# Optimization experiments

Measured on AMD Instinct MI355X. Metric: run time of the kernel, lower is better.

Reference implementation:

```python
import jax, jax.numpy as jnp
import numpy as np

IN_DIM = 16384; DM = 512; DEPTH = 4
DI = 1024   # d_inner = expand * d_model
DS = 16     # d_state
DC = 4      # d_conv
DR = 32     # dt_rank = ceil(d_model/16)
B = 4; L = 256


def setup_inputs() -> dict:
    key = jax.random.key(0)
    ks = jax.random.split(key, 12)
    g = lambda k, s, sc=0.02: jax.random.normal(k, s, jnp.float32) * sc
    return {
        "x": jax.random.normal(ks[0], (B, L, IN_DIM), jnp.float32),
        # top-level projections / norm
        "in_w": g(ks[1], (DM, IN_DIM)), "in_b": jnp.zeros((DM,), jnp.float32),
        "ln_g": jnp.ones((DM,), jnp.float32), "ln_b": jnp.zeros((DM,), jnp.float32),
        "out_w": g(ks[2], (IN_DIM, DM)), "out_b": jnp.zeros((IN_DIM,), jnp.float32),
        # stacked per-layer Mamba params (leading dim = DEPTH)
        "m_in_w": g(ks[3], (DEPTH, 2 * DI, DM)),
        "conv_w": g(ks[4], (DEPTH, DI, DC), 0.2),
        "conv_b": jnp.zeros((DEPTH, DI), jnp.float32),
        "xproj_w": g(ks[5], (DEPTH, DR + 2 * DS, DI)),
        "dt_w": g(ks[6], (DEPTH, DI, DR), 0.1),
        "dt_b": jax.random.uniform(ks[7], (DEPTH, DI), jnp.float32, -4.0, -2.0),
        "A_log": jnp.log(jnp.broadcast_to(jnp.arange(1, DS + 1, dtype=jnp.float32), (DEPTH, DI, DS))),
        "D_p": jnp.ones((DEPTH, DI), jnp.float32),
        "m_out_w": g(ks[8], (DEPTH, DM, DI)),
    }


def _mamba(h, iw, cw, cb, xw, dw, db, Alog, Dp, ow):
    """One Mamba block (no residual, matching bare mamba_ssm.Mamba)."""
    Bn, Ln, _ = h.shape
    xz = h @ iw.T                                  # [B,L,2*DI]
    xc, z = jnp.split(xz, 2, axis=-1)
    # causal depthwise conv1d, kernel DC, truncated to L
    xp = jnp.pad(xc, ((0, 0), (DC - 1, 0), (0, 0)))
    conv = cb
    for k in range(DC):
        conv = conv + xp[:, k:k + Ln, :] * cw[:, k]
    xc = jax.nn.silu(conv)                         # [B,L,DI]
    xdbl = xc @ xw.T                               # [B,L,DR+2*DS]
    dt, Bm, Cm = xdbl[..., :DR], xdbl[..., DR:DR + DS], xdbl[..., DR + DS:]
    dt = jax.nn.softplus(dt @ dw.T + db)           # [B,L,DI]
    A = -jnp.exp(Alog)                             # [DI,DS]
    dA = jnp.exp(dt[..., None] * A)                # [B,L,DI,DS]
    dBx = dt[..., None] * Bm[:, :, None, :] * xc[..., None]  # [B,L,DI,DS]

    def step(hst, inp):
        a, b, c = inp
        hst = a * hst + b
        return hst, jnp.einsum('bdn,bn->bd', hst, c)

    h0 = jnp.zeros((Bn, DI, DS), xc.dtype)
    _, ys = jax.lax.scan(step, h0, (dA.transpose(1, 0, 2, 3), dBx.transpose(1, 0, 2, 3), Cm.transpose(1, 0, 2)))
    y = ys.transpose(1, 0, 2) + xc * Dp            # [B,L,DI]
    y = y * jax.nn.silu(z)
    return y @ ow.T                                # [B,L,DM]


def reference(x, in_w, in_b, ln_g, ln_b, out_w, out_b, m_in_w, conv_w, conv_b, xproj_w, dt_w, dt_b, A_log, D_p, m_out_w):
    h = x @ in_w.T + in_b                          # [B,L,DM]
    for i in range(DEPTH):
        h = _mamba(h, m_in_w[i], conv_w[i], conv_b[i], xproj_w[i], dt_w[i], dt_b[i], A_log[i], D_p[i], m_out_w[i])
    hl = h[:, -1]                                  # [B,DM]
    mu = hl.mean(-1, keepdims=True)
    var = ((hl - mu) ** 2).mean(-1, keepdims=True)
    hn = (hl - mu) / jnp.sqrt(var + 1e-5) * ln_g + ln_b
    return hn @ out_w.T + out_b                    # [B,IN_DIM]
```

## Files before the change

### kernel.cpp

```cpp
#include <hip/hip_runtime.h>
#include <stdint.h>

#define DEV static __device__ __forceinline__

typedef __attribute__((ext_vector_type(8))) __bf16 bf16x8;
typedef __attribute__((ext_vector_type(4))) float f32x4;

DEV float bfs2f(unsigned short u) {
    union { unsigned int i; float f; } c; c.i = ((unsigned int)u) << 16; return c.f;
}
DEV unsigned short f2bf(float v) {
    union { __bf16 b; unsigned short u; } c; c.b = (__bf16)v; return c.u;
}

template<int TH, int BM, int BN, int BK, int AMODE, int BMODE, int EPI,
         int CSPLIT, int SWZ, int DBUF>
__global__ __launch_bounds__(TH) void gemm_k(
    const void* __restrict__ A0, const void* __restrict__ A1,
    const void* __restrict__ B0, const void* __restrict__ B1,
    const float* __restrict__ bias,
    float* __restrict__ C0, float* __restrict__ C1,
    int lda, int ldb, int ldc, int Klen, int pstride)
{
    constexpr int NWN = TH / 128;
    constexpr int FM = BM / 2 / 16;
    constexpr int FN = BN / NWN / 16;
    constexpr int KB = BK / 32;
    constexpr int GAF = (AMODE == 0) ? BM * BK / (TH * 4) : 1;
    constexpr int GAP = (AMODE == 1) ? BM * BK / (TH * 8) : 1;
    constexpr int GBF = (BMODE == 0) ? BN * BK / (TH * 4) : 1;
    constexpr int GBP = (BMODE == 1) ? BN * BK / (TH * 8) : 1;
    constexpr int BUFB = 2 * (BM + BN) * BK * 2;

    __shared__ __align__(16) char smem[(DBUF ? 2 : 1) * BUFB];

    int bx = blockIdx.x, by = blockIdx.y, bz = blockIdx.z;
    if (SWZ == 1) {
        int lin = blockIdx.x + gridDim.x * (blockIdx.y + gridDim.y * blockIdx.z);
        bz = lin & 7;
        int rest = lin >> 3;
        bx = rest % gridDim.x;
        by = rest / gridDim.x;
    } else if (SWZ == 2) {
        int lin = blockIdx.x + gridDim.x * blockIdx.y;
        int xcd = lin & 7, t = lin >> 3;
        int gpx = gridDim.y / 8;
        by = xcd * gpx + t % gpx;
        bx = t / gpx;
    }

    const int tid = threadIdx.x, lane = tid & 63;
    const int wid = tid >> 6;
    const int wm = wid & 1, wn = wid >> 1;
    const int q = lane >> 4, t16 = lane & 15;
    const int tileM = bx * BM, tileN = by * BN;
    const int kBase = bz * Klen, kEnd = kBase + Klen;
    float* C = C0 + (size_t)bz * pstride;

    f32x4 acc[FM][FN];
#pragma unroll
    for (int a = 0; a < FM; ++a)
#pragma unroll
        for (int b = 0; b < FN; ++b) acc[a][b] = f32x4{0.f, 0.f, 0.f, 0.f};

    float4 aF[GAF], bF[GBF];
    int4 aH[GAP], aL[GAP], bH[GBP], bL[GBP];

    auto loadA = [&](int k0) {
        if (AMODE == 0) {
            const float* A32 = (const float*)A0;
#pragma unroll
            for (int u = 0; u < GAF; ++u) {
                int idx = u * TH + tid;
                int r = idx / (BK / 4), c4 = idx % (BK / 4);
                aF[u] = *(const float4*)(A32 + (size_t)(tileM + r) * lda + k0 + c4 * 4);
            }
        } else {
            const unsigned short* Ah = (const unsigned short*)A0;
            const unsigned short* Al = (const unsigned short*)A1;
#pragma unroll
            for (int u = 0; u < GAP; ++u) {
                int idx = u * TH + tid;
                int r = idx / (BK / 8), c8 = idx % (BK / 8);
                size_t src = (size_t)(tileM + r) * lda + k0 + c8 * 8;
                aH[u] = *(const int4*)(Ah + src);
                aL[u] = *(const int4*)(Al + src);
            }
        }
    };
    auto loadB = [&](int k0) {
        if (BMODE == 0) {
            const float* B32 = (const float*)B0;
#pragma unroll
            for (int u = 0; u < GBF; ++u) {
                int idx = u * TH + tid;
                int r = idx / (BK / 4), c4 = idx % (BK / 4);
                bF[u] = *(const float4*)(B32 + (size_t)(tileN + r) * ldb + k0 + c4 * 4);
            }
        } else {
            const unsigned short* Bh = (const unsigned short*)B0;
            const unsigned short* Bl = (const unsigned short*)B1;
#pragma unroll
            for (int u = 0; u < GBP; ++u) {
                int idx = u * TH + tid;
                int r = idx / (BK / 8), c8 = idx % (BK / 8);
                size_t src = (size_t)(tileN + r) * ldb + k0 + c8 * 8;
                bH[u] = *(const int4*)(Bh + src);
                bL[u] = *(const int4*)(Bl + src);
            }
        }
    };
    auto storeA = [&](char* sAh, char* sAl) {
        if (AMODE == 0) {
#pragma unroll
            for (int u = 0; u < GAF; ++u) {
                int idx = u * TH + tid;
                int r = idx / (BK / 4), c4 = idx % (BK / 4);
                float vv[4] = {aF[u].x, aF[u].y, aF[u].z, aF[u].w};
                ushort4 hv, lv;
                unsigned short* hp = (unsigned short*)&hv;
                unsigned short* lp = (unsigned short*)&lv;
#pragma unroll
                for (int e = 0; e < 4; ++e) {
                    unsigned short hb = f2bf(vv[e]);
                    hp[e] = hb; lp[e] = f2bf(vv[e] - bfs2f(hb));
                }
                int off = (c4 / 8) * BM * 64 + r * 64 + (c4 & 7) * 8;
                *(ushort4*)(sAh + off) = hv;
                *(ushort4*)(sAl + off) = lv;
            }
        } else {
#pragma unroll
            for (int u = 0; u < GAP; ++u) {
                int idx = u * TH + tid;
                int r = idx / (BK / 8), c8 = idx % (BK / 8);
                int off = (c8 / 4) * BM * 64 + r * 64 + (c8 & 3) * 16;
                *(int4*)(sAh + off) = aH[u];
                *(int4*)(sAl + off) = aL[u];
            }
        }
    };
    auto storeB = [&](char* sBh, char* sBl) {
        if (BMODE == 0) {
#pragma unroll
            for (int u = 0; u < GBF; ++u) {
                int idx = u * TH + tid;
                int r = idx / (BK / 4), c4 = idx % (BK / 4);
                float vv[4] = {bF[u].x, bF[u].y, bF[u].z, bF[u].w};
                ushort4 hv, lv;
                unsigned short* hp = (unsigned short*)&hv;
                unsigned short* lp = (unsigned short*)&lv;
#pragma unroll
                for (int e = 0; e < 4; ++e) {
                    unsigned short hb = f2bf(vv[e]);
                    hp[e] = hb; lp[e] = f2bf(vv[e] - bfs2f(hb));
                }
                int off = (c4 / 8) * BN * 64 + r * 64 + (c4 & 7) * 8;
                *(ushort4*)(sBh + off) = hv;
                *(ushort4*)(sBl + off) = lv;
            }
        } else {
#pragma unroll
            for (int u = 0; u < GBP; ++u) {
                int idx = u * TH + tid;
                int r = idx / (BK / 8), c8 = idx % (BK / 8);
                int off = (c8 / 4) * BN * 64 + r * 64 + (c8 & 3) * 16;
                *(int4*)(sBh + off) = bH[u];
                *(int4*)(sBl + off) = bL[u];
            }
        }
    };
    auto compute = [&](const char* sAh, const char* sAl,
                       const char* sBh, const char* sBl) {
#pragma unroll
        for (int kb = 0; kb < KB; ++kb) {
            bf16x8 ah[FM], al[FM], bh[FN], bl[FN];
#pragma unroll
            for (int fm = 0; fm < FM; ++fm) {
                int off = kb * BM * 64 + (wm * (BM / 2) + fm * 16 + t16) * 64 + q * 16;
                ah[fm] = *(const bf16x8*)(sAh + off);
                al[fm] = *(const bf16x8*)(sAl + off);
            }
#pragma unroll
            for (int fn = 0; fn < FN; ++fn) {
                int off = kb * BN * 64 + (wn * (BN / NWN) + fn * 16 + t16) * 64 + q * 16;
                bh[fn] = *(const bf16x8*)(sBh + off);
                bl[fn] = *(const bf16x8*)(sBl + off);
            }
#pragma unroll
            for (int fm = 0; fm < FM; ++fm)
#pragma unroll
                for (int fn = 0; fn < FN; ++fn) {
                    acc[fm][fn] = __builtin_amdgcn_mfma_f32_16x16x32_bf16(ah[fm], bh[fn], acc[fm][fn], 0, 0, 0);
                    acc[fm][fn] = __builtin_amdgcn_mfma_f32_16x16x32_bf16(al[fm], bh[fn], acc[fm][fn], 0, 0, 0);
                    acc[fm][fn] = __builtin_amdgcn_mfma_f32_16x16x32_bf16(ah[fm], bl[fn], acc[fm][fn], 0, 0, 0);
                }
        }
    };

    loadA(kBase); loadB(kBase);
    if (DBUF) {
        storeA(smem, smem + BM * BK * 2);
        storeB(smem + 2 * BM * BK * 2, smem + 2 * BM * BK * 2 + BN * BK * 2);
        __syncthreads();
        int p = 0;
        for (int k0 = kBase; k0 < kEnd; k0 += BK) {
            bool more = (k0 + BK < kEnd);
            if (more) { loadA(k0 + BK); loadB(k0 + BK); }
            char* cb = smem + p * BUFB;
            compute(cb, cb + BM * BK * 2,
                    cb + 2 * BM * BK * 2, cb + 2 * BM * BK * 2 + BN * BK * 2);
            if (more) {
                char* nb = smem + (p ^ 1) * BUFB;
                storeA(nb, nb + BM * BK * 2);
                storeB(nb + 2 * BM * BK * 2, nb + 2 * BM * BK * 2 + BN * BK * 2);
            }
            __syncthreads();
            p ^= 1;
        }
    } else {
        for (int k0 = kBase; k0 < kEnd; k0 += BK) {
            storeA(smem, smem + BM * BK * 2);
            storeB(smem + 2 * BM * BK * 2, smem + 2 * BM * BK * 2 + BN * BK * 2);
            __syncthreads();
            if (k0 + BK < kEnd) { loadA(k0 + BK); loadB(k0 + BK); }
            compute(smem, smem + BM * BK * 2,
                    smem + 2 * BM * BK * 2, smem + 2 * BM * BK * 2 + BN * BK * 2);
            __syncthreads();
        }
    }

#pragma unroll
    for (int fm = 0; fm < FM; ++fm) {
        int row0 = tileM + wm * (BM / 2) + fm * 16 + q * 4;
#pragma unroll
        for (int fn = 0; fn < FN; ++fn) {
            int col = tileN + wn * (BN / NWN) + fn * 16 + t16;
            float* Cd = C; int cc2 = col;
            if (CSPLIT && col >= ldc) { Cd = C1; cc2 = col - ldc; }
            float bv = (EPI == 2) ? bias[col] : 0.f;
#pragma unroll
            for (int r = 0; r < 4; ++r) {
                float v = acc[fm][fn][r];
                if (EPI == 2) { v = fminf(v + bv, 60.f); v = log1pf(__expf(v)); }
                Cd[(size_t)(row0 + r) * ldc + cc2] = v;
            }
        }
    }
}

__global__ __launch_bounds__(256) void reduce_k(
    const float* __restrict__ part, int Z, int pstride, int n,
    const float* __restrict__ bias, int colmask,
    unsigned short* __restrict__ hi, unsigned short* __restrict__ lo,
    float* __restrict__ hlast, int colbits)
{
    int i = blockIdx.x * 256 + threadIdx.x;
    if (i >= n) return;
    float s = 0.f;
    for (int z = 0; z < Z; ++z) s += part[(size_t)z * pstride + i];
    if (bias) s += bias[i & colmask];
    unsigned short hb = f2bf(s);
    hi[i] = hb; lo[i] = f2bf(s - bfs2f(hb));
    if (hlast) {
        int row = i >> colbits;
        if ((row & 255) == 255)
            hlast[((row >> 8) << colbits) + (i & colmask)] = s;
    }
}

__global__ __launch_bounds__(256) void conv_silu_k(
    const float* __restrict__ xb, const float* __restrict__ cw,
    const float* __restrict__ cb, unsigned short* __restrict__ xch,
    unsigned short* __restrict__ xcl)
{
    int i  = blockIdx.x * 256 + threadIdx.x;
    int d  = i & 1023;
    int bl = i >> 10;
    int l  = bl & 255;
    float a = cb[d];
#pragma unroll
    for (int k = 0; k < 4; ++k) {
        int ls = l + k - 3;
        if (ls >= 0) a += xb[(size_t)(bl + k - 3) * 1024 + d] * cw[d * 4 + k];
    }
    float v = a / (1.f + __expf(-a));
    unsigned short hb = f2bf(v);
    xch[i] = hb; xcl[i] = f2bf(v - bfs2f(hb));
}

__global__ __launch_bounds__(256) void scan_k(
    const float* __restrict__ zb,
    const unsigned short* __restrict__ xch, const unsigned short* __restrict__ xcl,
    const unsigned short* __restrict__ xdh, const unsigned short* __restrict__ xdl,
    const float* __restrict__ dt, const float* __restrict__ Alog,
    const float* __restrict__ Dp,
    unsigned short* __restrict__ ygh, unsigned short* __restrict__ ygl)
{
    __shared__ float sdt[2048], sxc[2048], szz[2048], sbc[2048];
    int b   = blockIdx.x >> 5;
    int d0  = (blockIdx.x & 31) << 5;
    int ch  = threadIdx.x >> 3;
    int d   = d0 + ch;
    int sub = threadIdx.x & 7;
    int j0  = sub * 2;
    float An[2], hst[2] = {0.f, 0.f};
    An[0] = -__expf(Alog[d * 16 + j0]);
    An[1] = -__expf(Alog[d * 16 + j0 + 1]);
    float Dd  = Dp[d];
    int   bl0 = b * 256;

    for (int c = 0; c < 4; ++c) {
        __syncthreads();
#pragma unroll
        for (int it = 0; it < 8; ++it) {
            int j2 = it * 256 + threadIdx.x;
            int ll = j2 >> 5, dd = j2 & 31;
            size_t row = (size_t)(bl0 + c * 64 + ll);
            size_t gi  = row * 1024 + d0 + dd;
            sdt[j2] = dt[gi];
            sxc[j2] = bfs2f(xch[gi]) + bfs2f(xcl[gi]);
            szz[j2] = zb[gi];
            size_t bi = row * 64 + 32 + dd;
            sbc[j2] = bfs2f(xdh[bi]) + bfs2f(xdl[bi]);
        }
        __syncthreads();
#pragma unroll 4
        for (int li = 0; li < 64; ++li) {
            float dtv = sdt[li * 32 + ch];
            float xcv = sxc[li * 32 + ch];
            float c1  = dtv * xcv;
            float dA0 = __expf(dtv * An[0]);
            float dA1 = __expf(dtv * An[1]);
            float B0  = sbc[li * 32 + j0],      B1 = sbc[li * 32 + j0 + 1];
            float C0  = sbc[li * 32 + 16 + j0], C1 = sbc[li * 32 + 16 + j0 + 1];
            hst[0] = dA0 * hst[0] + c1 * B0;
            hst[1] = dA1 * hst[1] + c1 * B1;
            float y = hst[0] * C0 + hst[1] * C1;
            y += __shfl_xor(y, 1);
            y += __shfl_xor(y, 2);
            y += __shfl_xor(y, 4);
            if (sub == 0) {
                float zv = szz[li * 32 + ch];
                float sg = zv / (1.f + __expf(-zv));
                float v  = (y + xcv * Dd) * sg;
                unsigned short hb = f2bf(v);
                size_t o = (size_t)(bl0 + c * 64 + li) * 1024 + d;
                ygh[o] = hb; ygl[o] = f2bf(v - bfs2f(hb));
            }
        }
    }
}

__global__ __launch_bounds__(512) void ln_k(
    const float* __restrict__ hlast, const float* __restrict__ g,
    const float* __restrict__ bb, float* __restrict__ hn)
{
    __shared__ float red[16];
    int b = blockIdx.x, k = threadIdx.x;
    float x = hlast[b * 512 + k];
    float s = x, s2 = x * x;
#pragma unroll
    for (int m = 32; m; m >>= 1) { s += __shfl_xor(s, m, 64); s2 += __shfl_xor(s2, m, 64); }
    if ((k & 63) == 0) { red[k >> 6] = s; red[8 + (k >> 6)] = s2; }
    __syncthreads();
    float ts = 0.f, ts2 = 0.f;
#pragma unroll
    for (int j = 0; j < 8; ++j) { ts += red[j]; ts2 += red[8 + j]; }
    float mu   = ts * (1.f / 512.f);
    float var  = ts2 * (1.f / 512.f) - mu * mu;
    float rstd = rsqrtf(var + 1e-5f);
    hn[b * 512 + k] = (x - mu) * rstd * g[k] + bb[k];
}

__global__ __launch_bounds__(256) void final_k(
    const float* __restrict__ hn, const float* __restrict__ W,
    const float* __restrict__ ob, float* __restrict__ out)
{
    int wid = threadIdx.x >> 6, lane = threadIdx.x & 63;
    float a[4][8];
#pragma unroll
    for (int b2 = 0; b2 < 4; ++b2) {
        float4 v0 = *(const float4*)&hn[b2 * 512 + lane * 8];
        float4 v1 = *(const float4*)&hn[b2 * 512 + lane * 8 + 4];
        a[b2][0] = v0.x; a[b2][1] = v0.y; a[b2][2] = v0.z; a[b2][3] = v0.w;
        a[b2][4] = v1.x; a[b2][5] = v1.y; a[b2][6] = v1.z; a[b2][7] = v1.w;
    }
#pragma unroll 1
    for (int it = 0; it < 8; ++it) {
        int n = blockIdx.x * 4 + wid + it * 2048;
        const float* W32 = W + (size_t)n * 512 + lane * 8;
        float4 v0 = *(const float4*)W32;
        float4 v1 = *(const float4*)(W32 + 4);
        float wf[8] = {v0.x, v0.y, v0.z, v0.w, v1.x, v1.y, v1.z, v1.w};
        float s0 = 0.f, s1 = 0.f, s2 = 0.f, s3 = 0.f;
#pragma unroll
        for (int j = 0; j < 8; ++j) {
            s0 += a[0][j] * wf[j]; s1 += a[1][j] * wf[j];
            s2 += a[2][j] * wf[j]; s3 += a[3][j] * wf[j];
        }
#pragma unroll
        for (int m = 32; m; m >>= 1) {
            s0 += __shfl_xor(s0, m, 64); s1 += __shfl_xor(s1, m, 64);
            s2 += __shfl_xor(s2, m, 64); s3 += __shfl_xor(s3, m, 64);
        }
        if (lane == 0) {
            float bv = ob[n];
            out[0 * 16384 + n] = s0 + bv;
            out[1 * 16384 + n] = s1 + bv;
            out[2 * 16384 + n] = s2 + bv;
            out[3 * 16384 + n] = s3 + bv;
        }
    }
}

extern "C" void kernel_launch(void* const* d_in, const int* in_sizes, int n_in,
                              void* d_out, int out_size, void* d_ws, size_t ws_size,
                              hipStream_t stream)
{
    const float* x      = (const float*)d_in[0];
    const float* in_w   = (const float*)d_in[1];
    const float* in_b   = (const float*)d_in[2];
    const float* ln_g   = (const float*)d_in[3];
    const float* ln_b   = (const float*)d_in[4];
    const float* out_w  = (const float*)d_in[5];
    const float* out_b  = (const float*)d_in[6];
    const float* m_in_w = (const float*)d_in[7];
    const float* conv_w = (const float*)d_in[8];
    const float* conv_b = (const float*)d_in[9];
    const float* xproj_w= (const float*)d_in[10];
    const float* dt_w   = (const float*)d_in[11];
    const float* dt_b   = (const float*)d_in[12];
    const float* A_log  = (const float*)d_in[13];
    const float* D_p    = (const float*)d_in[14];
    const float* m_out_w= (const float*)d_in[15];

    char* W = (char*)d_ws;
    unsigned short* hplh = (unsigned short*)(W + 0);
    unsigned short* hpll = (unsigned short*)(W + 1048576);
    float* hlast = (float*)(W + 2097152);
    float* hn    = (float*)(W + 2162688);
    float* xbuf  = (float*)(W + 2228224);
    float* zbuf  = (float*)(W + 6422528);
    unsigned short* xch = (unsigned short*)(W + 10616832);
    unsigned short* xcl = (unsigned short*)(W + 12713984);
    float* dtb   = (float*)(W + 14811136);
    unsigned short* xdbh  = (unsigned short*)(W + 19005440);
    unsigned short* xdbl_ = (unsigned short*)(W + 19136512);
    float* part1 = (float*)(W + 2228224);
    float* partx = (float*)(W + 14811136);
    float* parto = (float*)(W + 6422528);
    unsigned short* ygh = (unsigned short*)(W + 2228224);
    unsigned short* ygl = (unsigned short*)(W + 4325376);

    gemm_k<512,128,128,64,0,0,0,0,1,1><<<dim3(8,4,8),512,0,stream>>>(
        x, nullptr, in_w, nullptr, nullptr, part1, nullptr,
        16384, 16384, 512, 2048, 524288);
    reduce_k<<<2048,256,0,stream>>>(part1, 8, 524288, 524288, in_b, 511,
                                    hplh, hpll, hlast, 9);

    for (int i = 0; i < 4; ++i) {
        const float* iw = m_in_w  + (size_t)i * 1048576;
        const float* cw = conv_w  + (size_t)i * 4096;
        const float* cb = conv_b  + (size_t)i * 1024;
        const float* xw = xproj_w + (size_t)i * 65536;
        const float* dw = dt_w    + (size_t)i * 32768;
        const float* db = dt_b    + (size_t)i * 1024;
        const float* Al = A_log   + (size_t)i * 16384;
        const float* Dp = D_p     + (size_t)i * 1024;
        const float* ow = m_out_w + (size_t)i * 524288;

        gemm_k<512,64,128,64,1,0,0,1,2,0><<<dim3(16,16,1),512,0,stream>>>(
            hplh, hpll, iw, nullptr, nullptr, xbuf, zbuf, 512, 512, 1024, 512, 0);
        conv_silu_k<<<4096,256,0,stream>>>(xbuf, cw, cb, xch, xcl);
        gemm_k<256,64,64,64,1,0,0,0,0,0><<<dim3(16,1,16),256,0,stream>>>(
            xch, xcl, xw, nullptr, nullptr, partx, nullptr, 1024, 1024, 64, 64, 65536);
        reduce_k<<<256,256,0,stream>>>(partx, 16, 65536, 65536, nullptr, 63,
                                       xdbh, xdbl_, nullptr, 6);
        gemm_k<256,64,64,32,1,0,2,0,0,0><<<dim3(16,16,1),256,0,stream>>>(
            xdbh, xdbl_, dw, nullptr, db, dtb, nullptr, 64, 32, 1024, 32, 0);
        scan_k<<<128,256,0,stream>>>(zbuf, xch, xcl, xdbh, xdbl_, dtb, Al, Dp,
                                     ygh, ygl);
        gemm_k<512,64,128,64,1,0,0,0,1,0><<<dim3(16,4,8),512,0,stream>>>(
            ygh, ygl, ow, nullptr, nullptr, parto, nullptr, 1024, 1024, 512, 128, 524288);
        reduce_k<<<2048,256,0,stream>>>(parto, 8, 524288, 524288, nullptr, 511,
                                        hplh, hpll, hlast, 9);
    }

    ln_k<<<4,512,0,stream>>>(hlast, ln_g, ln_b, hn);
    final_k<<<512,256,0,stream>>>(hn, out_w, out_b, (float*)d_out);
}
```

Measured before the change: 765.0 us.

## Prefetch next scan chunk into registers; drop GEMM block swizzles and double buffering

The selective-scan kernel now loads the next 64-step chunk of dt, x, z and B/C from global memory into registers while the current chunk is processed, then writes it to shared memory between barriers. The aim is to hide global load latency behind the serial recurrence. Separately, the XCD-aware block swizzles (SWZ 1/2) are turned off for the in-projection and out-projection GEMMs, and the first large GEMM no longer uses LDS double buffering. Those GEMM changes trade possible L2 locality and overlap for simpler indexing and lower LDS use.

```diff
diff --git a/kernel.cpp b/kernel.cpp
--- a/kernel.cpp
+++ b/kernel.cpp
@@ -41,12 +41,6 @@
         int rest = lin >> 3;
         bx = rest % gridDim.x;
         by = rest / gridDim.x;
-    } else if (SWZ == 2) {
-        int lin = blockIdx.x + gridDim.x * blockIdx.y;
-        int xcd = lin & 7, t = lin >> 3;
-        int gpx = gridDim.y / 8;
-        by = xcd * gpx + t % gpx;
-        bx = t / gpx;
     }
 
     const int tid = threadIdx.x, lane = tid & 63;
@@ -310,21 +304,38 @@
     float Dd  = Dp[d];
     int   bl0 = b * 256;
 
-    for (int c = 0; c < 4; ++c) {
-        __syncthreads();
+    float rdt[8], rzz[8];
+    unsigned short rxh[8], rxl[8], rbh[8], rbl[8];
+    auto stage_load = [&](int c) {
 #pragma unroll
         for (int it = 0; it < 8; ++it) {
             int j2 = it * 256 + threadIdx.x;
             int ll = j2 >> 5, dd = j2 & 31;
             size_t row = (size_t)(bl0 + c * 64 + ll);
             size_t gi  = row * 1024 + d0 + dd;
-            sdt[j2] = dt[gi];
-            sxc[j2] = bfs2f(xch[gi]) + bfs2f(xcl[gi]);
-            szz[j2] = zb[gi];
+            rdt[it] = dt[gi];
+            rxh[it] = xch[gi]; rxl[it] = xcl[gi];
+            rzz[it] = zb[gi];
             size_t bi = row * 64 + 32 + dd;
-            sbc[j2] = bfs2f(xdh[bi]) + bfs2f(xdl[bi]);
-        }
-        __syncthreads();
+            rbh[it] = xdh[bi]; rbl[it] = xdl[bi];
+        }
+    };
+    auto stage_write = [&]() {
+#pragma unroll
+        for (int it = 0; it < 8; ++it) {
+            int j2 = it * 256 + threadIdx.x;
+            sdt[j2] = rdt[it];
+            sxc[j2] = bfs2f(rxh[it]) + bfs2f(rxl[it]);
+            szz[j2] = rzz[it];
+            sbc[j2] = bfs2f(rbh[it]) + bfs2f(rbl[it]);
+        }
+    };
+
+    stage_load(0);
+    stage_write();
+    __syncthreads();
+    for (int c = 0; c < 4; ++c) {
+        if (c < 3) stage_load(c + 1);
 #pragma unroll 4
         for (int li = 0; li < 64; ++li) {
             float dtv = sdt[li * 32 + ch];
@@ -349,6 +360,11 @@
                 ygh[o] = hb; ygl[o] = f2bf(v - bfs2f(hb));
             }
         }
+        if (c < 3) {
+            __syncthreads();
+            stage_write();
+            __syncthreads();
+        }
     }
 }
 
@@ -453,7 +469,7 @@
     unsigned short* ygh = (unsigned short*)(W + 2228224);
     unsigned short* ygl = (unsigned short*)(W + 4325376);
 
-    gemm_k<512,128,128,64,0,0,0,0,1,1><<<dim3(8,4,8),512,0,stream>>>(
+    gemm_k<512,128,128,64,0,0,0,0,1,0><<<dim3(8,4,8),512,0,stream>>>(
         x, nullptr, in_w, nullptr, nullptr, part1, nullptr,
         16384, 16384, 512, 2048, 524288);
     reduce_k<<<2048,256,0,stream>>>(part1, 8, 524288, 524288, in_b, 511,
@@ -470,7 +486,7 @@
         const float* Dp = D_p     + (size_t)i * 1024;
         const float* ow = m_out_w + (size_t)i * 524288;
 
-        gemm_k<512,64,128,64,1,0,0,1,2,0><<<dim3(16,16,1),512,0,stream>>>(
+        gemm_k<512,64,128,64,1,0,0,1,0,0><<<dim3(16,16,1),512,0,stream>>>(
             hplh, hpll, iw, nullptr, nullptr, xbuf, zbuf, 512, 512, 1024, 512, 0);
         conv_silu_k<<<4096,256,0,stream>>>(xbuf, cw, cb, xch, xcl);
         gemm_k<256,64,64,64,1,0,0,0,0,0><<<dim3(16,1,16),256,0,stream>>>(
@@ -481,7 +497,7 @@
             xdbh, xdbl_, dw, nullptr, db, dtb, nullptr, 64, 32, 1024, 32, 0);
         scan_k<<<128,256,0,stream>>>(zbuf, xch, xcl, xdbh, xdbl_, dtb, Al, Dp,
                                      ygh, ygl);
-        gemm_k<512,64,128,64,1,0,0,0,1,0><<<dim3(16,4,8),512,0,stream>>>(
+        gemm_k<512,64,128,64,1,0,0,0,0,0><<<dim3(16,4,8),512,0,stream>>>(
             ygh, ygl, ow, nullptr, nullptr, parto, nullptr, 1024, 1024, 512, 128, 524288);
         reduce_k<<<2048,256,0,stream>>>(parto, 8, 524288, 524288, nullptr, 511,
                                         hplh, hpll, hlast, 9);
```

After: 772.1 us. Within noise of the previous version (+0.9%).
